# Optimization experiments

Measured on AMD Instinct MI355X. Metric: run time of the kernel, lower is better.

## Reference

```python
import jax, jax.numpy as jnp
import numpy as np

FP, DP, K, S, B, T, H, ZD = 96, 28, 3, 4, 64, 8, 512, 2
CP = FP - DP + 1          # 69, valid cross-correlation output size
NP = CP * CP              # 4761 = num_pixels


def setup_inputs() -> dict:
    key = jax.random.key(0)
    ks = jax.random.split(key, 12)
    def rn(k, shape, s=0.02):
        return jax.random.normal(k, shape, jnp.float32) * s
    return {
        "frames": jax.random.uniform(ks[0], (S, B, T, FP, FP), jnp.float32),
        "conv_kernel": jax.random.uniform(ks[1], (S, B, K, DP, DP), jnp.float32),
        "eps": jax.random.normal(ks[2], (S, B, K, ZD), jnp.float32),
        "W1": rn(ks[3], (NP, H)), "b1": jnp.zeros((H,), jnp.float32),
        "Wm1": rn(ks[4], (H, H // 2)), "bm1": jnp.zeros((H // 2,), jnp.float32),
        "Wm2": rn(ks[5], (H // 2, ZD)), "bm2": jnp.zeros((ZD,), jnp.float32),
        "Ws1": rn(ks[6], (H, H // 2)), "bs1": jnp.zeros((H // 2,), jnp.float32),
        "Ws2": rn(ks[7], (H // 2, ZD)), "bs2": jnp.zeros((ZD,), jnp.float32),
        "timestep": 0,
    }


def _axis_weights(p, n):
    """Bilinear 1-D gather indices/weights with zero padding outside [0, n)."""
    p0 = jnp.floor(p)
    f = p - p0
    i0 = p0.astype(jnp.int32)
    i1 = i0 + 1
    w0 = jnp.where((i0 >= 0) & (i0 < n), 1.0 - f, 0.0)
    w1 = jnp.where((i1 >= 0) & (i1 < n), f, 0.0)
    return jnp.clip(i0, 0, n - 1), jnp.clip(i1, 0, n - 1), w0, w1


def _place_digit(digit, zw):
    """AT.digit_to_frame: place DPxDP digit into FPxFP frame at z_where (torch
    affine_grid/grid_sample, align_corners=False, zero padding). theta scale =
    FP/DP, translation = -z_where*FP/DP, i.e. in_coord = (FP/DP)*(out - zw)."""
    scale = FP / DP
    out_c = (2.0 * jnp.arange(FP, dtype=jnp.float32) + 1.0) / FP - 1.0  # (FP,)
    px = ((scale * (out_c - zw[0]) + 1.0) * DP - 1.0) * 0.5  # x source pix
    py = ((scale * (out_c - zw[1]) + 1.0) * DP - 1.0) * 0.5  # y source pix
    y0, y1, wy0, wy1 = _axis_weights(py, DP)
    x0, x1, wx0, wx1 = _axis_weights(px, DP)
    # separable bilinear: interp rows then cols
    tmp = wy0[:, None] * digit[y0, :] + wy1[:, None] * digit[y1, :]  # (FP,DP)
    return wx0[None, :] * tmp[:, x0] + wx1[None, :] * tmp[:, x1]     # (FP,FP)

_place_batch = jax.vmap(_place_digit)


def reference(frames, conv_kernel, eps, W1, b1, Wm1, bm1, Wm2, bm2,
              Ws1, bs1, Ws2, bs2, timestep):
    SB = S * B
    frame_left = frames[:, :, timestep]  # (S,B,FP,FP)
    means, stds, zs = [], [], []
    for k in range(K):
        # per-sample dynamic-kernel cross-correlation via grouped conv
        lhs = frame_left.reshape(1, SB, FP, FP)
        rhs = conv_kernel[:, :, k].reshape(SB, 1, DP, DP)
        conved = jax.lax.conv_general_dilated(
            lhs, rhs, (1, 1), 'VALID', feature_group_count=SB)  # (1,SB,CP,CP)
        scores = jax.nn.softmax(conved.reshape(S, B, NP), axis=-1)
        h = jax.nn.relu(scores @ W1 + b1)                       # (S,B,H)
        mean_k = jnp.tanh(jax.nn.relu(h @ Wm1 + bm1) @ Wm2 + bm2)
        std_k = jnp.exp(jax.nn.relu(h @ Ws1 + bs1) @ Ws2 + bs2)
        z_k = mean_k + std_k * eps[:, :, k]                     # rsample
        recon = _place_batch(conv_kernel[:, :, k].reshape(SB, DP, DP),
                             z_k.reshape(SB, ZD)).reshape(S, B, FP, FP)
        frame_left = frame_left - recon
        means.append(mean_k); stds.append(std_k); zs.append(z_k)
    q_mean = jnp.stack(means, 2)    # (S,B,K,2)
    q_std = jnp.stack(stds, 2)
    z_where = jnp.stack(zs, 2)
    return jnp.stack([q_mean, q_std, z_where], 0)  # (3,S,B,K,2)
```

## Files before the change

kernel.cpp:

```cpp
#include <hip/hip_runtime.h>
#include <hip/hip_bf16.h>
#include <math.h>

#define FPD 96
#define DPD 28
#define CPD 69
#define NPD 4761
#define KKC 3
#define SBN 256
#define TT 8
#define HD 512
#define ZDD 2
#define KPAD 4768
#define SPLITK 15
#define FRSH 104
#define CVS 76

typedef __attribute__((ext_vector_type(8))) short bf16x8;
typedef __attribute__((ext_vector_type(4))) float f32x4;
typedef _Float16 half_t;
typedef __attribute__((ext_vector_type(2))) _Float16 half2_t;

__device__ __forceinline__ float bf2f_lo(unsigned int u) {
    union { unsigned int i; float f; } v; v.i = u << 16; return v.f;
}
__device__ __forceinline__ float bf2f_hi(unsigned int u) {
    union { unsigned int i; float f; } v; v.i = u & 0xffff0000u; return v.f;
}
__device__ __forceinline__ half2_t u2h(unsigned int u) {
    union { unsigned int i; half2_t h; } v; v.i = u; return v.h;
}

struct ConvLds {
    half_t fr[96 * FRSH];
    half_t kr[28 * 32];
    float  dg[2][784];
    float  cv[4][69 * CVS];
    float  red[32];
};

struct MlpLds {
    float hsh[HD];
    float h2[2][256];
    float res_sh[2][2];
};

__device__ __forceinline__ float recon_val(
    const float* __restrict__ dg, float zx, float zy, int r, int c)
{
    const float scale = 96.f / 28.f;
    float oci = (2.f * r + 1.f) / 96.f - 1.f;
    float ocj = (2.f * c + 1.f) / 96.f - 1.f;
    float py = ((scale * (oci - zy) + 1.f) * 28.f - 1.f) * 0.5f;
    float px = ((scale * (ocj - zx) + 1.f) * 28.f - 1.f) * 0.5f;
    float py0f = floorf(py), px0f = floorf(px);
    float fy = py - py0f, fx = px - px0f;
    int y0 = (int)py0f, x0 = (int)px0f;
    int y1 = y0 + 1, x1 = x0 + 1;
    float wy0 = (y0 >= 0 && y0 < DPD) ? 1.f - fy : 0.f;
    float wy1 = (y1 >= 0 && y1 < DPD) ? fy : 0.f;
    float wx0 = (x0 >= 0 && x0 < DPD) ? 1.f - fx : 0.f;
    float wx1 = (x1 >= 0 && x1 < DPD) ? fx : 0.f;
    int y0c = min(max(y0, 0), DPD - 1), y1c = min(max(y1, 0), DPD - 1);
    int x0c = min(max(x0, 0), DPD - 1), x1c = min(max(x1, 0), DPD - 1);
    float tmp0 = wy0 * dg[y0c * DPD + x0c] + wy1 * dg[y1c * DPD + x0c];
    float tmp1 = wy0 * dg[y0c * DPD + x1c] + wy1 * dg[y1c * DPD + x1c];
    return wx0 * tmp0 + wx1 * tmp1;
}

template<int NREC>
__device__ __forceinline__ void conv_rest(
    ConvLds& L, int ib, int t,
    const float* __restrict__ pf,
    float z0x, float z0y, float z1x, float z1y,
    ushort* __restrict__ e_buf, float* __restrict__ inv_denom)
{
    half_t* fr  = L.fr;
    half_t* kr  = L.kr;
    float*  red = L.red;

    #pragma unroll
    for (int i = 0; i < 9; ++i) {
        int p = t + i * 1024;
        int r = p / 96, c = p - r * 96;
        float val = pf[i];
        if (NREC >= 1) val -= recon_val(L.dg[0], z0x, z0y, r, c);
        if (NREC >= 2) val -= recon_val(L.dg[1], z1x, z1y, r, c);
        fr[r * FRSH + c] = (half_t)val;
    }
    if (t < 96 * 8) fr[(t >> 3) * FRSH + 96 + (t & 7)] = (half_t)0.f;
    __syncthreads();

    if (t < 828) {
        const int q    = t / 207;
        const int rem  = t - q * 207;
        const int tile = rem / 69;
        const int oy   = rem - tile * 69;
        const int ox0  = tile * 24;
        const int dy0  = q * 7;

        float acc[24];
        #pragma unroll
        for (int j = 0; j < 24; ++j) acc[j] = 0.f;

        #pragma unroll 1
        for (int dd = 0; dd < 7; ++dd) {
            const int dy = dy0 + dd;
            const unsigned int* frow = (const unsigned int*)&fr[(oy + dy) * FRSH + ox0];
            const unsigned int* krow = (const unsigned int*)&kr[dy * 32];
            unsigned int W[28], K[16], V[25];
            #pragma unroll
            for (int u = 0; u < 7; ++u) {
                uint4 v = *(const uint4*)(frow + 4 * u);
                W[4*u] = v.x; W[4*u+1] = v.y; W[4*u+2] = v.z; W[4*u+3] = v.w;
            }
            #pragma unroll
            for (int u = 0; u < 4; ++u) {
                uint4 v = *(const uint4*)(krow + 4 * u);
                K[4*u] = v.x; K[4*u+1] = v.y; K[4*u+2] = v.z; K[4*u+3] = v.w;
            }
            #pragma unroll
            for (int i = 0; i < 25; ++i)
                V[i] = (W[i] >> 16) | (W[i + 1] << 16);
            #pragma unroll
            for (int m = 0; m < 12; ++m) {
                float ae = acc[2*m], ao = acc[2*m+1];
                #pragma unroll
                for (int i = 0; i < 14; ++i) {
                    ae = __builtin_amdgcn_fdot2(u2h(W[m + i]), u2h(K[i]), ae, false);
                    ao = __builtin_amdgcn_fdot2(u2h(V[m + i]), u2h(K[i]), ao, false);
                }
                acc[2*m] = ae; acc[2*m+1] = ao;
            }
        }
        float* cvq = &L.cv[q][oy * CVS + ox0];
        #pragma unroll
        for (int u = 0; u < 6; ++u) {
            float4 v = make_float4(acc[4*u], acc[4*u+1], acc[4*u+2], acc[4*u+3]);
            *(float4*)(cvq + 4 * u) = v;
        }
    }
    __syncthreads();

    float m = -INFINITY;
    for (int p = t; p < 69 * CVS; p += 1024) {
        int ox = p - (p / CVS) * CVS;
        if (ox < CPD) {
            float v = L.cv[0][p] + L.cv[1][p] + L.cv[2][p] + L.cv[3][p];
            L.cv[0][p] = v;
            m = fmaxf(m, v);
        }
    }
    #pragma unroll
    for (int off = 32; off > 0; off >>= 1) m = fmaxf(m, __shfl_down(m, off, 64));
    int lane = t & 63, wid = t >> 6;
    if (lane == 0) red[wid] = m;
    __syncthreads();
    m = red[0];
    #pragma unroll
    for (int i = 1; i < 16; ++i) m = fmaxf(m, red[i]);

    float s = 0.f;
    ushort* eo = e_buf + (size_t)ib * KPAD;
    for (int p = t; p < 69 * CVS; p += 1024) {
        int oy = p / CVS;
        int ox = p - oy * CVS;
        if (ox < CPD) {
            float ev = __expf(L.cv[0][p] - m);
            __hip_bfloat16 h = __float2bfloat16(ev);
            eo[oy * CPD + ox] = *reinterpret_cast<ushort*>(&h);
            s += ev;
        }
    }
    #pragma unroll
    for (int off = 32; off > 0; off >>= 1) s += __shfl_down(s, off, 64);
    if (lane == 0) red[16 + wid] = s;
    __syncthreads();
    if (t == 0) {
        float tot = 0.f;
        #pragma unroll
        for (int i = 0; i < 16; ++i) tot += red[16 + i];
        inv_denom[ib] = 1.0f / tot;
    }
    if (t < KPAD - NPD) eo[NPD + t] = 0;
}

__device__ __forceinline__ void mlp_phase(
    MlpLds& L, int km, int ib, int t,
    float csum, float invd, float b1v,
    const ushort* __restrict__ WhidT,
    const float* __restrict__ bm1, const float* __restrict__ bs1,
    const float* __restrict__ Wm2, const float* __restrict__ bm2,
    const float* __restrict__ Ws2, const float* __restrict__ bs2,
    const float* __restrict__ eps, float* __restrict__ out,
    float* z_keep)
{
    if (t < HD)
        L.hsh[t] = fmaxf(fmaf(csum, invd, b1v), 0.f);
    __syncthreads();

    if (t < 512) {
        int head = t >> 8, col = t & 255;
        const uint4* Wr = (const uint4*)(WhidT + (size_t)(head * 256 + col) * 512);
        float bias = head ? bs1[col] : bm1[col];
        float a = 0.f;
        #pragma unroll 8
        for (int u = 0; u < 64; ++u) {
            uint4 wv = Wr[u];
            const float* hp = &L.hsh[u * 8];
            a = fmaf(hp[0], bf2f_lo(wv.x), a);
            a = fmaf(hp[1], bf2f_hi(wv.x), a);
            a = fmaf(hp[2], bf2f_lo(wv.y), a);
            a = fmaf(hp[3], bf2f_hi(wv.y), a);
            a = fmaf(hp[4], bf2f_lo(wv.z), a);
            a = fmaf(hp[5], bf2f_hi(wv.z), a);
            a = fmaf(hp[6], bf2f_lo(wv.w), a);
            a = fmaf(hp[7], bf2f_hi(wv.w), a);
        }
        L.h2[head][col] = fmaxf(a + bias, 0.f);
    }
    __syncthreads();

    {
        int w = t >> 6, l = t & 63;
        if (w < 4) {
            int zd = (w >> 1) & 1, head = w & 1;
            const float* W2 = head ? Ws2 : Wm2;
            float a = 0.f;
            #pragma unroll
            for (int u = 0; u < 4; ++u) {
                int i = l + u * 64;
                a = fmaf(L.h2[head][i], W2[i * 2 + zd], a);
            }
            #pragma unroll
            for (int off = 32; off > 0; off >>= 1) a += __shfl_down(a, off, 64);
            if (l == 0) {
                float r = head ? __expf(a + bs2[zd]) : tanhf(a + bm2[zd]);
                L.res_sh[zd][head] = r;
            }
        }
    }
    __syncthreads();
    if (t < 2) {
        int zd = t;
        float mean = L.res_sh[zd][0];
        float stdv = L.res_sh[zd][1];
        float ev = eps[(size_t)ib * 6 + km * 2 + zd];
        float z = fmaf(stdv, ev, mean);
        int oidx = ib * 6 + km * 2 + zd;
        out[oidx]        = mean;
        out[1536 + oidx] = stdv;
        out[3072 + oidx] = z;
        z_keep[zd] = z;
    }
}

__global__
__attribute__((amdgpu_flat_work_group_size(1024, 1024)))
__attribute__((amdgpu_waves_per_eu(4, 4)))
void conv0_wprep_kernel(
    const float* __restrict__ frames, const int* __restrict__ tsp,
    const float* __restrict__ ck,
    ushort* __restrict__ e_buf, float* __restrict__ inv_denom,
    const float* __restrict__ W1, const float* __restrict__ Wm1,
    const float* __restrict__ Ws1,
    ushort* __restrict__ W1T, ushort* __restrict__ WhidT)
{
    __shared__ union __align__(16) {
        ConvLds conv;
        ushort wp[4][64][65];
    } sh;
    const int t  = threadIdx.x;
    const int ib = blockIdx.x;

    const float* src = frames + ((size_t)ib * TT + *tsp) * 9216;
    float pf[9];
    #pragma unroll
    for (int i = 0; i < 9; ++i) pf[i] = src[t + i * 1024];
    if (t < 28 * 32) {
        int dy = t >> 5, dx = t & 31;
        float v = (dx < 28) ? ck[((size_t)ib * KKC + 0) * 784 + dy * 28 + dx] : 0.f;
        sh.conv.kr[t] = (half_t)v;
    }

    conv_rest<0>(sh.conv, ib, t, pf, 0.f, 0.f, 0.f, 0.f, e_buf, inv_denom);
    __syncthreads();

    {
        const int g  = t >> 8;
        const int tt = t & 255;
        const int ln = tt & 63;
        const int lr = tt >> 6;
        const int b  = ib * 4 + g;
        ushort (*tile)[65] = sh.wp[g];

        if (b < 600) {
            const int k0 = (b % 75) * 64;
            const int n0 = (b / 75) * 64;
            #pragma unroll
            for (int i = 0; i < 16; ++i) {
                int kk = k0 + lr + i * 4;
                float v = (kk < NPD) ? W1[(size_t)kk * HD + n0 + ln] : 0.f;
                __hip_bfloat16 h = __float2bfloat16(v);
                tile[lr + i * 4][ln] = *reinterpret_cast<ushort*>(&h);
            }
        } else if (b < 664) {
            const int bb = b - 600;
            const int i0 = (bb & 7) * 64;
            const int r0 = (bb >> 3) * 64;
            #pragma unroll
            for (int rep = 0; rep < 16; ++rep) {
                int i = i0 + lr + rep * 4;
                int r = r0 + ln;
                const float* srcp = (r >= 256) ? Ws1 : Wm1;
                float v = srcp[(size_t)i * 256 + (r & 255)];
                __hip_bfloat16 h = __float2bfloat16(v);
                tile[lr + rep * 4][ln] = *reinterpret_cast<ushort*>(&h);
            }
        }
        __syncthreads();
        if (b < 600) {
            const int k0 = (b % 75) * 64;
            const int n0 = (b / 75) * 64;
            #pragma unroll
            for (int i = 0; i < 16; ++i) {
                int nn = lr + i * 4;
                int kk = k0 + ln;
                if (kk < KPAD)
                    W1T[(size_t)(n0 + nn) * KPAD + kk] = tile[ln][nn];
            }
        } else if (b < 664) {
            const int bb = b - 600;
            const int i0 = (bb & 7) * 64;
            const int r0 = (bb >> 3) * 64;
            #pragma unroll
            for (int rep = 0; rep < 16; ++rep) {
                int r = r0 + lr + rep * 4;
                WhidT[(size_t)r * 512 + i0 + ln] = tile[ln][lr + rep * 4];
            }
        }
    }
}

#define GLOADSET(A,B0,B1,B2,B3,OFF)                        \
    A  = *(const bf16x8*)(pA + (OFF));                     \
    B0 = *(const bf16x8*)(pB + (OFF));                     \
    B1 = *(const bf16x8*)(pB + 16 * KPAD + (OFF));         \
    B2 = *(const bf16x8*)(pB + 32 * KPAD + (OFF));         \
    B3 = *(const bf16x8*)(pB + 48 * KPAD + (OFF));

__global__ __launch_bounds__(64) void gemm1_mfma(
    const ushort* __restrict__ E, const ushort* __restrict__ W1T,
    float* __restrict__ Cpart)
{
    const int t  = threadIdx.x;
    const int bx = blockIdx.x;
    const int n0 = blockIdx.y * 64;
    const int z  = blockIdx.z;
    const int step0 = z * 10;
    const int nstep = min(10, 149 - step0);

    const int lm = t & 15;
    const int kb = (t & 63) >> 4;

    f32x4 zero = {0.f, 0.f, 0.f, 0.f};
    f32x4 acc[4] = {zero, zero, zero, zero};

    const ushort* pA = E   + (size_t)(bx * 16 + lm) * KPAD + kb * 8;
    const ushort* pB = W1T + (size_t)(n0 + lm) * KPAD + kb * 8;
    const int kk0 = step0 * 32;

    bf16x8 a0, b00, b01, b02, b03;
    bf16x8 a1, b10, b11, b12, b13;
    GLOADSET(a0, b00, b01, b02, b03, kk0)
    GLOADSET(a1, b10, b11, b12, b13, kk0 + 32)

    int s = 0;
    for (; s + 2 <= nstep; s += 2) {
        bf16x8 ca = a0, c0 = b00, c1 = b01, c2 = b02, c3 = b03;
        if (s + 2 < nstep) { int kn = kk0 + (s + 2) * 32;
            GLOADSET(a0, b00, b01, b02, b03, kn) }
        acc[0] = __builtin_amdgcn_mfma_f32_16x16x32_bf16(ca, c0, acc[0], 0, 0, 0);
        acc[1] = __builtin_amdgcn_mfma_f32_16x16x32_bf16(ca, c1, acc[1], 0, 0, 0);
        acc[2] = __builtin_amdgcn_mfma_f32_16x16x32_bf16(ca, c2, acc[2], 0, 0, 0);
        acc[3] = __builtin_amdgcn_mfma_f32_16x16x32_bf16(ca, c3, acc[3], 0, 0, 0);

        bf16x8 da = a1, d0 = b10, d1 = b11, d2 = b12, d3 = b13;
        if (s + 3 < nstep) { int kn = kk0 + (s + 3) * 32;
            GLOADSET(a1, b10, b11, b12, b13, kn) }
        acc[0] = __builtin_amdgcn_mfma_f32_16x16x32_bf16(da, d0, acc[0], 0, 0, 0);
        acc[1] = __builtin_amdgcn_mfma_f32_16x16x32_bf16(da, d1, acc[1], 0, 0, 0);
        acc[2] = __builtin_amdgcn_mfma_f32_16x16x32_bf16(da, d2, acc[2], 0, 0, 0);
        acc[3] = __builtin_amdgcn_mfma_f32_16x16x32_bf16(da, d3, acc[3], 0, 0, 0);
    }
    if (s < nstep) {
        acc[0] = __builtin_amdgcn_mfma_f32_16x16x32_bf16(a0, b00, acc[0], 0, 0, 0);
        acc[1] = __builtin_amdgcn_mfma_f32_16x16x32_bf16(a0, b01, acc[1], 0, 0, 0);
        acc[2] = __builtin_amdgcn_mfma_f32_16x16x32_bf16(a0, b02, acc[2], 0, 0, 0);
        acc[3] = __builtin_amdgcn_mfma_f32_16x16x32_bf16(a0, b03, acc[3], 0, 0, 0);
    }

    const int mrow = bx * 16 + kb * 4;
    #pragma unroll
    for (int j = 0; j < 4; ++j) {
        int n = n0 + j * 16 + lm;
        #pragma unroll
        for (int rg = 0; rg < 4; ++rg)
            Cpart[((size_t)(mrow + rg) * SPLITK + z) * HD + n] = acc[j][rg];
    }
}

template<int KM>
__global__
__attribute__((amdgpu_flat_work_group_size(1024, 1024)))
__attribute__((amdgpu_waves_per_eu(4, 4)))
void mlp_conv_kernel(
    const float* __restrict__ Cpart, const float* __restrict__ inv_denom,
    const float* __restrict__ b1, const ushort* __restrict__ WhidT,
    const float* __restrict__ bm1, const float* __restrict__ bs1,
    const float* __restrict__ Wm2, const float* __restrict__ bm2,
    const float* __restrict__ Ws2, const float* __restrict__ bs2,
    const float* __restrict__ eps, float* __restrict__ out,
    const float* __restrict__ frames, const int* __restrict__ tsp,
    const float* __restrict__ ck, ushort* __restrict__ e_buf)
{
    __shared__ union __align__(16) {
        ConvLds conv;
        MlpLds  mlp;
    } sh;
    __shared__ float z_keep[2];
    const int t  = threadIdx.x;
    const int ib = blockIdx.x;

    const float* src = frames + ((size_t)ib * TT + *tsp) * 9216;
    float pf[9];
    #pragma unroll
    for (int i = 0; i < 9; ++i) pf[i] = src[t + i * 1024];
    if (t < 28 * 32) {
        int dy = t >> 5, dx = t & 31;
        float v = (dx < 28)
            ? ck[((size_t)ib * KKC + (KM + 1)) * 784 + dy * 28 + dx] : 0.f;
        sh.conv.kr[t] = (half_t)v;
    }
    if (t < 784) {
        sh.conv.dg[0][t] = ck[((size_t)ib * KKC + 0) * 784 + t];
        if (KM == 1)
            sh.conv.dg[1][t] = ck[((size_t)ib * KKC + 1) * 784 + t];
    }
    float z0x = 0.f, z0y = 0.f;
    if (KM == 1) {
        z0x = out[3072 + ib * 6 + 0];
        z0y = out[3072 + ib * 6 + 1];
    }
    float csum = 0.f, b1v = 0.f;
    if (t < HD) {
        #pragma unroll
        for (int z = 0; z < SPLITK; ++z)
            csum += Cpart[((size_t)ib * SPLITK + z) * HD + t];
        b1v = b1[t];
    }
    float invd = inv_denom[ib];

    mlp_phase(sh.mlp, KM, ib, t, csum, invd, b1v, WhidT,
              bm1, bs1, Wm2, bm2, Ws2, bs2, eps, out, z_keep);
    __syncthreads();

    float zkx = z_keep[0], zky = z_keep[1];
    if (KM == 0) {
        conv_rest<1>(sh.conv, ib, t, pf, zkx, zky, 0.f, 0.f,
                     e_buf, (float*)inv_denom);
    } else {
        conv_rest<2>(sh.conv, ib, t, pf, z0x, z0y, zkx, zky,
                     e_buf, (float*)inv_denom);
    }
}

__global__ __launch_bounds__(512) void mlp_final_kernel(
    const float* __restrict__ Cpart, const float* __restrict__ inv_denom,
    const float* __restrict__ b1, const ushort* __restrict__ WhidT,
    const float* __restrict__ bm1, const float* __restrict__ bs1,
    const float* __restrict__ Wm2, const float* __restrict__ bm2,
    const float* __restrict__ Ws2, const float* __restrict__ bs2,
    const float* __restrict__ eps, float* __restrict__ out)
{
    __shared__ MlpLds L;
    __shared__ float z_keep[2];
    const int t  = threadIdx.x;
    const int ib = blockIdx.x;
    float csum = 0.f, b1v = 0.f;
    if (t < HD) {
        #pragma unroll
        for (int z = 0; z < SPLITK; ++z)
            csum += Cpart[((size_t)ib * SPLITK + z) * HD + t];
        b1v = b1[t];
    }
    float invd = inv_denom[ib];
    mlp_phase(L, 2, ib, t, csum, invd, b1v, WhidT,
              bm1, bs1, Wm2, bm2, Ws2, bs2, eps, out, z_keep);
}

extern "C" void kernel_launch(void* const* d_in, const int* in_sizes, int n_in,
                              void* d_out, int out_size, void* d_ws, size_t ws_size,
                              hipStream_t stream)
{
    const float* frames = (const float*)d_in[0];
    const float* ck     = (const float*)d_in[1];
    const float* eps    = (const float*)d_in[2];
    const float* W1     = (const float*)d_in[3];
    const float* b1     = (const float*)d_in[4];
    const float* Wm1    = (const float*)d_in[5];
    const float* bm1    = (const float*)d_in[6];
    const float* Wm2    = (const float*)d_in[7];
    const float* bm2    = (const float*)d_in[8];
    const float* Ws1    = (const float*)d_in[9];
    const float* bs1    = (const float*)d_in[10];
    const float* Ws2    = (const float*)d_in[11];
    const float* bs2    = (const float*)d_in[12];
    const int*   tsp    = (const int*)d_in[13];
    float* out = (float*)d_out;

    float* Cpart   = (float*)d_ws;
    float* inv_den = Cpart + 1966080;
    ushort* e_buf  = (ushort*)(inv_den + 256);
    ushort* W1T    = e_buf + (size_t)SBN * KPAD;
    ushort* WhidT  = W1T + (size_t)HD * KPAD;

    conv0_wprep_kernel<<<256, 1024, 0, stream>>>(
        frames, tsp, ck, e_buf, inv_den, W1, Wm1, Ws1, W1T, WhidT);
    gemm1_mfma<<<dim3(16, 8, SPLITK), 64, 0, stream>>>(e_buf, W1T, Cpart);
    mlp_conv_kernel<0><<<256, 1024, 0, stream>>>(
        Cpart, inv_den, b1, WhidT, bm1, bs1, Wm2, bm2, Ws2, bs2,
        eps, out, frames, tsp, ck, e_buf);
    gemm1_mfma<<<dim3(16, 8, SPLITK), 64, 0, stream>>>(e_buf, W1T, Cpart);
    mlp_conv_kernel<1><<<256, 1024, 0, stream>>>(
        Cpart, inv_den, b1, WhidT, bm1, bs1, Wm2, bm2, Ws2, bs2,
        eps, out, frames, tsp, ck, e_buf);
    gemm1_mfma<<<dim3(16, 8, SPLITK), 64, 0, stream>>>(e_buf, W1T, Cpart);
    mlp_final_kernel<<<256, 512, 0, stream>>>(
        Cpart, inv_den, b1, WhidT, bm1, bs1, Wm2, bm2, Ws2, bs2, eps, out);
}
```

Before: 305.3 us.

## Split each sample's conv/softmax across two blocks with split-softmax merge

Each sample's cross-correlation and softmax now runs as two blocks, each covering half the output rows, so 512 blocks are launched instead of 256. Each half writes its local max and exp-sum, and the MLP stage merges them by rescaling the split-K GEMM partial sums from each K-half. The K dimension is repadded to two 2560-element halves so the GEMM split is an even 16 steps and needs no tail. The cost is redundant MLP work in both halves of the block pair, duplicated frame-row loads, more padded GEMM work, and extra exp rescaling.

Result: slower. 335.7 us (+10.0%).

```diff
diff --git a/kernel.cpp b/kernel.cpp
--- a/kernel.cpp
+++ b/kernel.cpp
@@ -11,8 +11,9 @@
 #define TT 8
 #define HD 512
 #define ZDD 2
-#define KPAD 4768
-#define SPLITK 15
+#define KP2 5120
+#define HALFK 2560
+#define SPLITK 16
 #define FRSH 104
 #define CVS 76
 
@@ -32,10 +33,10 @@
 }
 
 struct ConvLds {
-    half_t fr[96 * FRSH];
+    half_t fr[62 * FRSH];
     half_t kr[28 * 32];
     float  dg[2][784];
-    float  cv[4][69 * CVS];
+    float  cv[4][35 * CVS];
     float  red[32];
 };
 
@@ -68,34 +69,51 @@
     return wx0 * tmp0 + wx1 * tmp1;
 }
 
+__device__ __forceinline__ void stage_kernel_rows(
+    ConvLds& L, const float* __restrict__ ck, int ib, int k, int t)
+{
+    if (t < 28 * 32) {
+        int dy = t >> 5, dx = t & 31;
+        float v = (dx < 28) ? ck[((size_t)ib * KKC + k) * 784 + dy * 28 + dx] : 0.f;
+        L.kr[t] = (half_t)v;
+    }
+}
+
 template<int NREC>
 __device__ __forceinline__ void conv_rest(
-    ConvLds& L, int ib, int t,
+    ConvLds& L, int ib, int half, int t,
     const float* __restrict__ pf,
     float z0x, float z0y, float z1x, float z1y,
-    ushort* __restrict__ e_buf, float* __restrict__ inv_denom)
+    ushort* __restrict__ e_buf, float* __restrict__ stats_w)
 {
     half_t* fr  = L.fr;
-    half_t* kr  = L.kr;
     float*  red = L.red;
-
-    #pragma unroll
-    for (int i = 0; i < 9; ++i) {
+    const int roy0  = half ? 35 : 0;
+    const int nrows = half ? 61 : 62;
+    const int oycnt = half ? 34 : 35;
+    const int lim   = nrows * 96;
+
+    #pragma unroll
+    for (int i = 0; i < 6; ++i) {
         int p = t + i * 1024;
-        int r = p / 96, c = p - r * 96;
-        float val = pf[i];
-        if (NREC >= 1) val -= recon_val(L.dg[0], z0x, z0y, r, c);
-        if (NREC >= 2) val -= recon_val(L.dg[1], z1x, z1y, r, c);
-        fr[r * FRSH + c] = (half_t)val;
-    }
-    if (t < 96 * 8) fr[(t >> 3) * FRSH + 96 + (t & 7)] = (half_t)0.f;
-    __syncthreads();
-
-    if (t < 828) {
-        const int q    = t / 207;
-        const int rem  = t - q * 207;
-        const int tile = rem / 69;
-        const int oy   = rem - tile * 69;
+        if (p < lim) {
+            int lr = p / 96, c = p - lr * 96;
+            int r = roy0 + lr;
+            float val = pf[i];
+            if (NREC >= 1) val -= recon_val(L.dg[0], z0x, z0y, r, c);
+            if (NREC >= 2) val -= recon_val(L.dg[1], z1x, z1y, r, c);
+            fr[lr * FRSH + c] = (half_t)val;
+        }
+    }
+    if (t < 62 * 8) fr[(t >> 3) * FRSH + 96 + (t & 7)] = (half_t)0.f;
+    __syncthreads();
+
+    const int NT = 12 * oycnt;
+    if (t < NT) {
+        const int q    = t / (3 * oycnt);
+        const int rem  = t - q * (3 * oycnt);
+        const int tile = rem / oycnt;
+        const int oyl  = rem - tile * oycnt;
         const int ox0  = tile * 24;
         const int dy0  = q * 7;
 
@@ -106,8 +124,8 @@
         #pragma unroll 1
         for (int dd = 0; dd < 7; ++dd) {
             const int dy = dy0 + dd;
-            const unsigned int* frow = (const unsigned int*)&fr[(oy + dy) * FRSH + ox0];
-            const unsigned int* krow = (const unsigned int*)&kr[dy * 32];
+            const unsigned int* frow = (const unsigned int*)&fr[(oyl + dy) * FRSH + ox0];
+            const unsigned int* krow = (const unsigned int*)&L.kr[dy * 32];
             unsigned int W[28], K[16], V[25];
             #pragma unroll
             for (int u = 0; u < 7; ++u) {
@@ -133,7 +151,7 @@
                 acc[2*m] = ae; acc[2*m+1] = ao;
             }
         }
-        float* cvq = &L.cv[q][oy * CVS + ox0];
+        float* cvq = &L.cv[q][oyl * CVS + ox0];
         #pragma unroll
         for (int u = 0; u < 6; ++u) {
             float4 v = make_float4(acc[4*u], acc[4*u+1], acc[4*u+2], acc[4*u+3]);
@@ -142,8 +160,9 @@
     }
     __syncthreads();
 
+    const int nele = oycnt * CVS;
     float m = -INFINITY;
-    for (int p = t; p < 69 * CVS; p += 1024) {
+    for (int p = t; p < nele; p += 1024) {
         int ox = p - (p / CVS) * CVS;
         if (ox < CPD) {
             float v = L.cv[0][p] + L.cv[1][p] + L.cv[2][p] + L.cv[3][p];
@@ -160,15 +179,16 @@
     #pragma unroll
     for (int i = 1; i < 16; ++i) m = fmaxf(m, red[i]);
 
+    const int kbase = half ? HALFK : 0;
     float s = 0.f;
-    ushort* eo = e_buf + (size_t)ib * KPAD;
-    for (int p = t; p < 69 * CVS; p += 1024) {
-        int oy = p / CVS;
-        int ox = p - oy * CVS;
+    ushort* eo = e_buf + (size_t)ib * KP2;
+    for (int p = t; p < nele; p += 1024) {
+        int oyl = p / CVS;
+        int ox = p - oyl * CVS;
         if (ox < CPD) {
             float ev = __expf(L.cv[0][p] - m);
             __hip_bfloat16 h = __float2bfloat16(ev);
-            eo[oy * CPD + ox] = *reinterpret_cast<ushort*>(&h);
+            eo[kbase + oyl * 69 + ox] = *reinterpret_cast<ushort*>(&h);
             s += ev;
         }
     }
@@ -180,9 +200,12 @@
         float tot = 0.f;
         #pragma unroll
         for (int i = 0; i < 16; ++i) tot += red[16 + i];
-        inv_denom[ib] = 1.0f / tot;
-    }
-    if (t < KPAD - NPD) eo[NPD + t] = 0;
+        stats_w[ib * 4 + half * 2]     = m;
+        stats_w[ib * 4 + half * 2 + 1] = tot;
+    }
+    const int padbase = half ? (HALFK + 34 * 69) : (35 * 69);
+    const int padcnt  = half ? (KP2 - (HALFK + 34 * 69)) : (HALFK - 35 * 69);
+    if (t < padcnt) eo[padbase + t] = 0;
 }
 
 __device__ __forceinline__ void mlp_phase(
@@ -255,13 +278,34 @@
     }
 }
 
-__global__
-__attribute__((amdgpu_flat_work_group_size(1024, 1024)))
-__attribute__((amdgpu_waves_per_eu(4, 4)))
-void conv0_wprep_kernel(
+__device__ __forceinline__ void mlp_inputs(
+    const float* __restrict__ Cpart, const float* __restrict__ stats_r,
+    const float* __restrict__ b1, int ib, int t,
+    float& csum, float& invd, float& b1v)
+{
+    float c0 = 0.f, c1 = 0.f;
+    b1v = 0.f;
+    if (t < HD) {
+        #pragma unroll
+        for (int z = 0; z < 8; ++z)
+            c0 += Cpart[((size_t)ib * SPLITK + z) * HD + t];
+        #pragma unroll
+        for (int z = 8; z < 16; ++z)
+            c1 += Cpart[((size_t)ib * SPLITK + z) * HD + t];
+        b1v = b1[t];
+    }
+    float M0 = stats_r[ib * 4 + 0], S0 = stats_r[ib * 4 + 1];
+    float M1 = stats_r[ib * 4 + 2], S1 = stats_r[ib * 4 + 3];
+    float M  = fmaxf(M0, M1);
+    float f0 = __expf(M0 - M), f1 = __expf(M1 - M);
+    invd = 1.f / fmaf(S0, f0, S1 * f1);
+    csum = fmaf(c0, f0, c1 * f1);
+}
+
+__global__ __launch_bounds__(1024, 8) void conv0_wprep_kernel(
     const float* __restrict__ frames, const int* __restrict__ tsp,
     const float* __restrict__ ck,
-    ushort* __restrict__ e_buf, float* __restrict__ inv_denom,
+    ushort* __restrict__ e_buf, float* __restrict__ stats0,
     const float* __restrict__ W1, const float* __restrict__ Wm1,
     const float* __restrict__ Ws1,
     ushort* __restrict__ W1T, ushort* __restrict__ WhidT)
@@ -270,20 +314,24 @@
         ConvLds conv;
         ushort wp[4][64][65];
     } sh;
-    const int t  = threadIdx.x;
-    const int ib = blockIdx.x;
-
-    const float* src = frames + ((size_t)ib * TT + *tsp) * 9216;
-    float pf[9];
-    #pragma unroll
-    for (int i = 0; i < 9; ++i) pf[i] = src[t + i * 1024];
-    if (t < 28 * 32) {
-        int dy = t >> 5, dx = t & 31;
-        float v = (dx < 28) ? ck[((size_t)ib * KKC + 0) * 784 + dy * 28 + dx] : 0.f;
-        sh.conv.kr[t] = (half_t)v;
-    }
-
-    conv_rest<0>(sh.conv, ib, t, pf, 0.f, 0.f, 0.f, 0.f, e_buf, inv_denom);
+    const int t    = threadIdx.x;
+    const int ibh  = blockIdx.x;
+    const int ib   = ibh >> 1;
+    const int half = ibh & 1;
+
+    const int roy0 = half ? 35 : 0;
+    const int lim  = (half ? 61 : 62) * 96;
+    const float* src = frames + ((size_t)ib * TT + *tsp) * 9216 + roy0 * 96;
+    float pf[6];
+    #pragma unroll
+    for (int i = 0; i < 6; ++i) {
+        int p = t + i * 1024;
+        pf[i] = (p < lim) ? src[p] : 0.f;
+    }
+    stage_kernel_rows(sh.conv, ck, ib, 0, t);
+    __syncthreads();
+
+    conv_rest<0>(sh.conv, ib, half, t, pf, 0.f, 0.f, 0.f, 0.f, e_buf, stats0);
     __syncthreads();
 
     {
@@ -291,21 +339,23 @@
         const int tt = t & 255;
         const int ln = tt & 63;
         const int lr = tt >> 6;
-        const int b  = ib * 4 + g;
+        const int b  = ibh * 4 + g;
         ushort (*tile)[65] = sh.wp[g];
 
-        if (b < 600) {
-            const int k0 = (b % 75) * 64;
-            const int n0 = (b / 75) * 64;
+        if (b < 640) {
+            const int k0 = (b % 80) * 64;
+            const int n0 = (b / 80) * 64;
             #pragma unroll
             for (int i = 0; i < 16; ++i) {
                 int kk = k0 + lr + i * 4;
-                float v = (kk < NPD) ? W1[(size_t)kk * HD + n0 + ln] : 0.f;
+                int np = (kk < HALFK) ? kk : kk - 145;
+                bool ok = (kk < 2415) || (kk >= HALFK && kk < 4906);
+                float v = ok ? W1[(size_t)np * HD + n0 + ln] : 0.f;
                 __hip_bfloat16 h = __float2bfloat16(v);
                 tile[lr + i * 4][ln] = *reinterpret_cast<ushort*>(&h);
             }
-        } else if (b < 664) {
-            const int bb = b - 600;
+        } else if (b < 704) {
+            const int bb = b - 640;
             const int i0 = (bb & 7) * 64;
             const int r0 = (bb >> 3) * 64;
             #pragma unroll
@@ -319,18 +369,17 @@
             }
         }
         __syncthreads();
-        if (b < 600) {
-            const int k0 = (b % 75) * 64;
-            const int n0 = (b / 75) * 64;
+        if (b < 640) {
+            const int k0 = (b % 80) * 64;
+            const int n0 = (b / 80) * 64;
             #pragma unroll
             for (int i = 0; i < 16; ++i) {
                 int nn = lr + i * 4;
                 int kk = k0 + ln;
-                if (kk < KPAD)
-                    W1T[(size_t)(n0 + nn) * KPAD + kk] = tile[ln][nn];
-            }
-        } else if (b < 664) {
-            const int bb = b - 600;
+                W1T[(size_t)(n0 + nn) * KP2 + kk] = tile[ln][nn];
+            }
+        } else if (b < 704) {
+            const int bb = b - 640;
             const int i0 = (bb & 7) * 64;
             const int r0 = (bb >> 3) * 64;
             #pragma unroll
@@ -345,9 +394,9 @@
 #define GLOADSET(A,B0,B1,B2,B3,OFF)                        \
     A  = *(const bf16x8*)(pA + (OFF));                     \
     B0 = *(const bf16x8*)(pB + (OFF));                     \
-    B1 = *(const bf16x8*)(pB + 16 * KPAD + (OFF));         \
-    B2 = *(const bf16x8*)(pB + 32 * KPAD + (OFF));         \
-    B3 = *(const bf16x8*)(pB + 48 * KPAD + (OFF));
+    B1 = *(const bf16x8*)(pB + 16 * KP2 + (OFF));          \
+    B2 = *(const bf16x8*)(pB + 32 * KP2 + (OFF));          \
+    B3 = *(const bf16x8*)(pB + 48 * KP2 + (OFF));
 
 __global__ __launch_bounds__(64) void gemm1_mfma(
     const ushort* __restrict__ E, const ushort* __restrict__ W1T,
@@ -357,8 +406,6 @@
     const int bx = blockIdx.x;
     const int n0 = blockIdx.y * 64;
     const int z  = blockIdx.z;
-    const int step0 = z * 10;
-    const int nstep = min(10, 149 - step0);
 
     const int lm = t & 15;
     const int kb = (t & 63) >> 4;
@@ -366,19 +413,19 @@
     f32x4 zero = {0.f, 0.f, 0.f, 0.f};
     f32x4 acc[4] = {zero, zero, zero, zero};
 
-    const ushort* pA = E   + (size_t)(bx * 16 + lm) * KPAD + kb * 8;
-    const ushort* pB = W1T + (size_t)(n0 + lm) * KPAD + kb * 8;
-    const int kk0 = step0 * 32;
+    const ushort* pA = E   + (size_t)(bx * 16 + lm) * KP2 + kb * 8;
+    const ushort* pB = W1T + (size_t)(n0 + lm) * KP2 + kb * 8;
+    const int kk0 = z * 320;
 
     bf16x8 a0, b00, b01, b02, b03;
     bf16x8 a1, b10, b11, b12, b13;
     GLOADSET(a0, b00, b01, b02, b03, kk0)
     GLOADSET(a1, b10, b11, b12, b13, kk0 + 32)
 
-    int s = 0;
-    for (; s + 2 <= nstep; s += 2) {
+    #pragma unroll 1
+    for (int s = 0; s < 10; s += 2) {
         bf16x8 ca = a0, c0 = b00, c1 = b01, c2 = b02, c3 = b03;
-        if (s + 2 < nstep) { int kn = kk0 + (s + 2) * 32;
+        if (s + 2 < 10) { int kn = kk0 + (s + 2) * 32;
             GLOADSET(a0, b00, b01, b02, b03, kn) }
         acc[0] = __builtin_amdgcn_mfma_f32_16x16x32_bf16(ca, c0, acc[0], 0, 0, 0);
         acc[1] = __builtin_amdgcn_mfma_f32_16x16x32_bf16(ca, c1, acc[1], 0, 0, 0);
@@ -386,19 +433,13 @@
         acc[3] = __builtin_amdgcn_mfma_f32_16x16x32_bf16(ca, c3, acc[3], 0, 0, 0);
 
         bf16x8 da = a1, d0 = b10, d1 = b11, d2 = b12, d3 = b13;
-        if (s + 3 < nstep) { int kn = kk0 + (s + 3) * 32;
+        if (s + 3 < 10) { int kn = kk0 + (s + 3) * 32;
             GLOADSET(a1, b10, b11, b12, b13, kn) }
         acc[0] = __builtin_amdgcn_mfma_f32_16x16x32_bf16(da, d0, acc[0], 0, 0, 0);
         acc[1] = __builtin_amdgcn_mfma_f32_16x16x32_bf16(da, d1, acc[1], 0, 0, 0);
         acc[2] = __builtin_amdgcn_mfma_f32_16x16x32_bf16(da, d2, acc[2], 0, 0, 0);
         acc[3] = __builtin_amdgcn_mfma_f32_16x16x32_bf16(da, d3, acc[3], 0, 0, 0);
     }
-    if (s < nstep) {
-        acc[0] = __builtin_amdgcn_mfma_f32_16x16x32_bf16(a0, b00, acc[0], 0, 0, 0);
-        acc[1] = __builtin_amdgcn_mfma_f32_16x16x32_bf16(a0, b01, acc[1], 0, 0, 0);
-        acc[2] = __builtin_amdgcn_mfma_f32_16x16x32_bf16(a0, b02, acc[2], 0, 0, 0);
-        acc[3] = __builtin_amdgcn_mfma_f32_16x16x32_bf16(a0, b03, acc[3], 0, 0, 0);
-    }
 
     const int mrow = bx * 16 + kb * 4;
     #pragma unroll
@@ -411,11 +452,9 @@
 }
 
 template<int KM>
-__global__
-__attribute__((amdgpu_flat_work_group_size(1024, 1024)))
-__attribute__((amdgpu_waves_per_eu(4, 4)))
-void mlp_conv_kernel(
-    const float* __restrict__ Cpart, const float* __restrict__ inv_denom,
+__global__ __launch_bounds__(1024, 8) void mlp_conv_kernel(
+    const float* __restrict__ Cpart, const float* __restrict__ stats_r,
+    float* __restrict__ stats_w,
     const float* __restrict__ b1, const ushort* __restrict__ WhidT,
     const float* __restrict__ bm1, const float* __restrict__ bs1,
     const float* __restrict__ Wm2, const float* __restrict__ bm2,
@@ -429,19 +468,21 @@
         MlpLds  mlp;
     } sh;
     __shared__ float z_keep[2];
-    const int t  = threadIdx.x;
-    const int ib = blockIdx.x;
-
-    const float* src = frames + ((size_t)ib * TT + *tsp) * 9216;
-    float pf[9];
-    #pragma unroll
-    for (int i = 0; i < 9; ++i) pf[i] = src[t + i * 1024];
-    if (t < 28 * 32) {
-        int dy = t >> 5, dx = t & 31;
-        float v = (dx < 28)
-            ? ck[((size_t)ib * KKC + (KM + 1)) * 784 + dy * 28 + dx] : 0.f;
-        sh.conv.kr[t] = (half_t)v;
-    }
+    const int t    = threadIdx.x;
+    const int ibh  = blockIdx.x;
+    const int ib   = ibh >> 1;
+    const int half = ibh & 1;
+
+    const int roy0 = half ? 35 : 0;
+    const int lim  = (half ? 61 : 62) * 96;
+    const float* src = frames + ((size_t)ib * TT + *tsp) * 9216 + roy0 * 96;
+    float pf[6];
+    #pragma unroll
+    for (int i = 0; i < 6; ++i) {
+        int p = t + i * 1024;
+        pf[i] = (p < lim) ? src[p] : 0.f;
+    }
+    stage_kernel_rows(sh.conv, ck, ib, KM + 1, t);
     if (t < 784) {
         sh.conv.dg[0][t] = ck[((size_t)ib * KKC + 0) * 784 + t];
         if (KM == 1)
@@ -452,14 +493,8 @@
         z0x = out[3072 + ib * 6 + 0];
         z0y = out[3072 + ib * 6 + 1];
     }
-    float csum = 0.f, b1v = 0.f;
-    if (t < HD) {
-        #pragma unroll
-        for (int z = 0; z < SPLITK; ++z)
-            csum += Cpart[((size_t)ib * SPLITK + z) * HD + t];
-        b1v = b1[t];
-    }
-    float invd = inv_denom[ib];
+    float csum, invd, b1v;
+    mlp_inputs(Cpart, stats_r, b1, ib, t, csum, invd, b1v);
 
     mlp_phase(sh.mlp, KM, ib, t, csum, invd, b1v, WhidT,
               bm1, bs1, Wm2, bm2, Ws2, bs2, eps, out, z_keep);
@@ -467,16 +502,16 @@
 
     float zkx = z_keep[0], zky = z_keep[1];
     if (KM == 0) {
-        conv_rest<1>(sh.conv, ib, t, pf, zkx, zky, 0.f, 0.f,
-                     e_buf, (float*)inv_denom);
+        conv_rest<1>(sh.conv, ib, half, t, pf, zkx, zky, 0.f, 0.f,
+                     e_buf, stats_w);
     } else {
-        conv_rest<2>(sh.conv, ib, t, pf, z0x, z0y, zkx, zky,
-                     e_buf, (float*)inv_denom);
+        conv_rest<2>(sh.conv, ib, half, t, pf, z0x, z0y, zkx, zky,
+                     e_buf, stats_w);
     }
 }
 
 __global__ __launch_bounds__(512) void mlp_final_kernel(
-    const float* __restrict__ Cpart, const float* __restrict__ inv_denom,
+    const float* __restrict__ Cpart, const float* __restrict__ stats_r,
     const float* __restrict__ b1, const ushort* __restrict__ WhidT,
     const float* __restrict__ bm1, const float* __restrict__ bs1,
     const float* __restrict__ Wm2, const float* __restrict__ bm2,
@@ -487,14 +522,8 @@
     __shared__ float z_keep[2];
     const int t  = threadIdx.x;
     const int ib = blockIdx.x;
-    float csum = 0.f, b1v = 0.f;
-    if (t < HD) {
-        #pragma unroll
-        for (int z = 0; z < SPLITK; ++z)
-            csum += Cpart[((size_t)ib * SPLITK + z) * HD + t];
-        b1v = b1[t];
-    }
-    float invd = inv_denom[ib];
+    float csum, invd, b1v;
+    mlp_inputs(Cpart, stats_r, b1, ib, t, csum, invd, b1v);
     mlp_phase(L, 2, ib, t, csum, invd, b1v, WhidT,
               bm1, bs1, Wm2, bm2, Ws2, bs2, eps, out, z_keep);
 }
@@ -520,22 +549,23 @@
     float* out = (float*)d_out;
 
     float* Cpart   = (float*)d_ws;
-    float* inv_den = Cpart + 1966080;
-    ushort* e_buf  = (ushort*)(inv_den + 256);
-    ushort* W1T    = e_buf + (size_t)SBN * KPAD;
-    ushort* WhidT  = W1T + (size_t)HD * KPAD;
-
-    conv0_wprep_kernel<<<256, 1024, 0, stream>>>(
-        frames, tsp, ck, e_buf, inv_den, W1, Wm1, Ws1, W1T, WhidT);
+    float* statsA  = Cpart + 2097152;
+    float* statsB  = statsA + 1024;
+    ushort* e_buf  = (ushort*)(statsB + 1024);
+    ushort* W1T    = e_buf + (size_t)SBN * KP2;
+    ushort* WhidT  = W1T + (size_t)HD * KP2;
+
+    conv0_wprep_kernel<<<512, 1024, 0, stream>>>(
+        frames, tsp, ck, e_buf, statsA, W1, Wm1, Ws1, W1T, WhidT);
     gemm1_mfma<<<dim3(16, 8, SPLITK), 64, 0, stream>>>(e_buf, W1T, Cpart);
-    mlp_conv_kernel<0><<<256, 1024, 0, stream>>>(
-        Cpart, inv_den, b1, WhidT, bm1, bs1, Wm2, bm2, Ws2, bs2,
+    mlp_conv_kernel<0><<<512, 1024, 0, stream>>>(
+        Cpart, statsA, statsB, b1, WhidT, bm1, bs1, Wm2, bm2, Ws2, bs2,
         eps, out, frames, tsp, ck, e_buf);
     gemm1_mfma<<<dim3(16, 8, SPLITK), 64, 0, stream>>>(e_buf, W1T, Cpart);
-    mlp_conv_kernel<1><<<256, 1024, 0, stream>>>(
-        Cpart, inv_den, b1, WhidT, bm1, bs1, Wm2, bm2, Ws2, bs2,
+    mlp_conv_kernel<1><<<512, 1024, 0, stream>>>(
+        Cpart, statsB, statsA, b1, WhidT, bm1, bs1, Wm2, bm2, Ws2, bs2,
         eps, out, frames, tsp, ck, e_buf);
     gemm1_mfma<<<dim3(16, 8, SPLITK), 64, 0, stream>>>(e_buf, W1T, Cpart);
     mlp_final_kernel<<<256, 512, 0, stream>>>(
-        Cpart, inv_den, b1, WhidT, bm1, bs1, Wm2, bm2, Ws2, bs2, eps, out);
-}
+        Cpart, statsA, b1, WhidT, bm1, bs1, Wm2, bm2, Ws2, bs2, eps, out);
+}
```
